# Performance work log

Measured on AMD Instinct MI355X. Metric: run time of the kernel, lower is better.

Reference implementation:

```python
import jax, jax.numpy as jnp
import numpy as np

B, S, D, H = 2, 2048, 1024, 16
DK = D // H


def setup_inputs() -> dict:
    key = jax.random.key(0)
    ks = jax.random.split(key, 12)
    scale = 1.0 / np.sqrt(D)
    inp = {
        "query": jax.random.normal(ks[0], (B, S, D), jnp.float32),
        "key": jax.random.normal(ks[1], (B, S, D), jnp.float32),
        "value": jax.random.normal(ks[2], (B, S, D), jnp.float32),
        "mask": jnp.broadcast_to(jnp.tril(jnp.ones((S, S), bool)), (B, S, S)),
        "Wq": jax.random.normal(ks[3], (D, D), jnp.float32) * scale,
        "bq": jnp.zeros((D,), jnp.float32),
        "Wk": jax.random.normal(ks[4], (D, D), jnp.float32) * scale,
        "bk": jnp.zeros((D,), jnp.float32),
        "Wv": jax.random.normal(ks[5], (D, D), jnp.float32) * scale,
        "bv": jnp.zeros((D,), jnp.float32),
        "Wo": jax.random.normal(ks[6], (D, D), jnp.float32) * scale,
        "bo": jnp.zeros((D,), jnp.float32),
    }
    return inp


def _split_heads(x):
    # [B, S, D] -> [B, H, S, DK]
    return x.reshape(B, S, H, DK).transpose(0, 2, 1, 3)


def reference(query, key, value, mask, Wq, bq, Wk, bk, Wv, bv, Wo, bo):
    q = _split_heads(query @ Wq + bq)
    k = _split_heads(key @ Wk + bk)
    v = _split_heads(value @ Wv + bv)
    # scores: [B, H, S, S]
    scores = jnp.einsum("bhqd,bhkd->bhqk", q, k) / jnp.sqrt(jnp.float32(DK))
    scores = jnp.where(mask[:, None, :, :], scores, jnp.float32(-1e9))
    p_attn = jax.nn.softmax(scores, axis=-1)
    x = jnp.einsum("bhqk,bhkd->bhqd", p_attn, v)  # [B, H, S, DK]
    x = x.transpose(0, 2, 1, 3).reshape(B, S, D)
    return x @ Wo + bo
```

## Files before the change

### kernel.cpp

```cpp
#include <hip/hip_runtime.h>


#define S_LEN 2048
#define DMODEL 1024
#define NHEAD 16
#define DKH 64
#define QSCALE 0.18033688011112042f

typedef __attribute__((ext_vector_type(8))) short short8;
typedef __attribute__((ext_vector_type(4))) float f32x4;
typedef __attribute__((ext_vector_type(4))) unsigned short ushort4v;

__device__ __forceinline__ unsigned short f2bf(float f) {
  union { float f; unsigned int u; } v; v.f = f;
  unsigned int r = v.u + 0x7fffu + ((v.u >> 16) & 1u);
  return (unsigned short)(r >> 16);
}

__device__ __forceinline__ void gload_lds16(const void* g, void* l) {
  __builtin_amdgcn_global_load_lds(
      (const __attribute__((address_space(1))) void*)g,
      (__attribute__((address_space(3))) void*)l, 16, 0, 0);
}

__global__ __launch_bounds__(256) void transpose_cast(const float* __restrict__ W,
                                                      unsigned short* __restrict__ Wt) {
  __shared__ float tile[32][33];
  const int tx = threadIdx.x, ty = threadIdx.y;
  const int c0 = blockIdx.x * 32, r0 = blockIdx.y * 32;
#pragma unroll
  for (int i = 0; i < 32; i += 8)
    tile[ty + i][tx] = W[(r0 + ty + i) * 1024 + c0 + tx];
  __syncthreads();
#pragma unroll
  for (int i = 0; i < 32; i += 8)
    Wt[(c0 + ty + i) * 1024 + r0 + tx] = f2bf(tile[tx][ty + i]);
}

__global__ __launch_bounds__(256) void cast3(const float* __restrict__ s0,
                                             const float* __restrict__ s1,
                                             const float* __restrict__ s2,
                                             unsigned short* __restrict__ d0,
                                             unsigned short* __restrict__ d1,
                                             unsigned short* __restrict__ d2) {
  const int z = blockIdx.y;
  const float* src = (z == 0) ? s0 : (z == 1) ? s1 : s2;
  unsigned short* dst = (z == 0) ? d0 : (z == 1) ? d1 : d2;
  const int i = (blockIdx.x * 256 + threadIdx.x) * 8;
  float4 a = *(const float4*)&src[i];
  float4 b = *(const float4*)&src[i + 4];
  unsigned short u[8];
  u[0] = f2bf(a.x); u[1] = f2bf(a.y); u[2] = f2bf(a.z); u[3] = f2bf(a.w);
  u[4] = f2bf(b.x); u[5] = f2bf(b.y); u[6] = f2bf(b.z); u[7] = f2bf(b.w);
  *(short8*)&dst[i] = *(short8*)u;
}

__global__ __launch_bounds__(256) void qkv_gemm(
    const unsigned short* Qc, const unsigned short* Kc, const unsigned short* Vc,
    const unsigned short* WtQ, const unsigned short* WtK, const unsigned short* WtV,
    const float* bq, const float* bk, const float* bv,
    unsigned short* Qw, unsigned short* Kw, unsigned short* Vtw) {
  __shared__ unsigned short Alds[2][4096];
  __shared__ unsigned short Blds[2][4096];
  const int z = blockIdx.z;
  const unsigned short* A  = (z == 0) ? Qc : (z == 1) ? Kc : Vc;
  const unsigned short* Wt = (z == 0) ? WtQ : (z == 1) ? WtK : WtV;
  const float* bias        = (z == 0) ? bq : (z == 1) ? bk : bv;

  const int tid = threadIdx.x;
  const int m0 = blockIdx.x * 128, n0 = blockIdx.y * 128;
  const int wid = tid >> 6, lane = tid & 63;
  const int lg = lane >> 4, lr = lane & 15;
  const int wr = (wid >> 1) * 64, wc = (wid & 1) * 64;
  const int srow_base = wid * 32 + (lane >> 2);
  const int scol = (lane & 3) * 8;

  f32x4 acc[4][4] = {};

#define GSTAGE(BUF, KT)                                                          \
  {                                                                              \
    _Pragma("unroll")                                                            \
    for (int i = 0; i < 2; i++) {                                                \
      const int row = srow_base + i * 16;                                        \
      gload_lds16(A  + (m0 + row) * 1024 + (KT) + scol,                          \
                  (char*)&Alds[BUF][0] + wid * 2048 + i * 1024);                 \
      gload_lds16(Wt + (n0 + row) * 1024 + (KT) + scol,                          \
                  (char*)&Blds[BUF][0] + wid * 2048 + i * 1024);                 \
    }                                                                            \
  }

  GSTAGE(0, 0)
  int cur = 0;
  for (int kt = 0; kt < 1024; kt += 32) {
    __syncthreads();
    if (kt + 32 < 1024) GSTAGE(cur ^ 1, kt + 32)
    short8 af[4], bfr[4];
#pragma unroll
    for (int i = 0; i < 4; i++) af[i] = *(short8*)&Alds[cur][(wr + i * 16 + lr) * 32 + lg * 8];
#pragma unroll
    for (int i = 0; i < 4; i++) bfr[i] = *(short8*)&Blds[cur][(wc + i * 16 + lr) * 32 + lg * 8];
#pragma unroll
    for (int mi = 0; mi < 4; mi++)
#pragma unroll
      for (int ni = 0; ni < 4; ni++)
        acc[mi][ni] = __builtin_amdgcn_mfma_f32_16x16x32_bf16(af[mi], bfr[ni], acc[mi][ni], 0, 0, 0);
    cur ^= 1;
  }
#undef GSTAGE

  if (z < 2) {
    unsigned short* O = (z == 0) ? Qw : Kw;
    const float sc = (z == 0) ? QSCALE : 1.0f;
#pragma unroll
    for (int mi = 0; mi < 4; mi++)
#pragma unroll
      for (int ni = 0; ni < 4; ni++) {
        const int gn = n0 + wc + ni * 16 + lr;
        const int h = gn >> 6, dk = gn & 63;
        const float bb = bias[gn];
#pragma unroll
        for (int r = 0; r < 4; r++) {
          const int gm = m0 + wr + mi * 16 + lg * 4 + r;
          const int b = gm >> 11, s = gm & 2047;
          O[(((b * NHEAD + h) * S_LEN + s) << 6) + dk] = f2bf((acc[mi][ni][r] + bb) * sc);
        }
      }
  } else {
#pragma unroll
    for (int mi = 0; mi < 4; mi++)
#pragma unroll
      for (int ni = 0; ni < 4; ni++) {
        const int gn = n0 + wc + ni * 16 + lr;
        const int h = gn >> 6, dk = gn & 63;
        const float bb = bias[gn];
        const int gm = m0 + wr + mi * 16 + lg * 4;
        const int b = gm >> 11, s = gm & 2047;
        unsigned short u[4];
#pragma unroll
        for (int r = 0; r < 4; r++) u[r] = f2bf(acc[mi][ni][r] + bb);
        *(ushort4v*)&Vtw[(((b * NHEAD + h) * DKH + dk) << 11) + s] = *(ushort4v*)u;
      }
  }
}

__global__ __launch_bounds__(256) void oproj_gemm(const unsigned short* __restrict__ A,
                                                  const unsigned short* __restrict__ Wt,
                                                  const float* __restrict__ bias,
                                                  float* __restrict__ Of32) {
  __shared__ unsigned short Alds[2][2048];
  __shared__ unsigned short Blds[2][4096];
  const int tid = threadIdx.x;
  const int m0 = blockIdx.x * 64, n0 = blockIdx.y * 128;
  const int wid = tid >> 6, lane = tid & 63;
  const int lg = lane >> 4, lr = lane & 15;
  const int wc = wid * 32;
  const int arow = wid * 16 + (lane >> 2);
  const int brow_base = wid * 32 + (lane >> 2);
  const int scol = (lane & 3) * 8;

  f32x4 acc[4][2] = {};

#define OSTAGE(BUF, KT)                                                          \
  {                                                                              \
    gload_lds16(A + (m0 + arow) * 1024 + (KT) + scol,                            \
                (char*)&Alds[BUF][0] + wid * 1024);                              \
    _Pragma("unroll")                                                            \
    for (int i = 0; i < 2; i++) {                                                \
      const int row = brow_base + i * 16;                                        \
      gload_lds16(Wt + (n0 + row) * 1024 + (KT) + scol,                          \
                  (char*)&Blds[BUF][0] + wid * 2048 + i * 1024);                 \
    }                                                                            \
  }

  OSTAGE(0, 0)
  int cur = 0;
  for (int kt = 0; kt < 1024; kt += 32) {
    __syncthreads();
    if (kt + 32 < 1024) OSTAGE(cur ^ 1, kt + 32)
    short8 af[4], bfr[2];
#pragma unroll
    for (int i = 0; i < 4; i++) af[i] = *(short8*)&Alds[cur][(i * 16 + lr) * 32 + lg * 8];
#pragma unroll
    for (int j = 0; j < 2; j++) bfr[j] = *(short8*)&Blds[cur][(wc + j * 16 + lr) * 32 + lg * 8];
#pragma unroll
    for (int mi = 0; mi < 4; mi++)
#pragma unroll
      for (int ni = 0; ni < 2; ni++)
        acc[mi][ni] = __builtin_amdgcn_mfma_f32_16x16x32_bf16(af[mi], bfr[ni], acc[mi][ni], 0, 0, 0);
    cur ^= 1;
  }
#undef OSTAGE

#pragma unroll
  for (int mi = 0; mi < 4; mi++)
#pragma unroll
    for (int ni = 0; ni < 2; ni++) {
      const int gn = n0 + wc + ni * 16 + lr;
      const float bb = bias[gn];
#pragma unroll
      for (int r = 0; r < 4; r++) {
        const int gm = m0 + mi * 16 + lg * 4 + r;
        Of32[gm * 1024 + gn] = acc[mi][ni][r] + bb;
      }
    }
}

__global__ __launch_bounds__(256) void attn_k(const unsigned short* __restrict__ Q,
                                              const unsigned short* __restrict__ K,
                                              const unsigned short* __restrict__ Vt,
                                              unsigned short* __restrict__ X) {
  __shared__ unsigned short Kb[2][4096];
  __shared__ unsigned short Vb[2][4096];
  __shared__ unsigned short Plds[4][16][72];
  const int tid = threadIdx.x;
  const int wid = tid >> 6, lane = tid & 63;
  const int lg = lane >> 4, lr = lane & 15;
  const int bh = blockIdx.y;
  const unsigned short* Qh = Q + bh * (S_LEN * DKH);
  const char* KhB = (const char*)(K + bh * (S_LEN * DKH));
  const char* VtB = (const char*)(Vt + bh * (DKH * S_LEN));
  const int b = bh >> 4, h = bh & 15;

  const int srow_lo = (lane >> 3);
  const int scolb = (lane & 7) * 16;

  short8 ones8;
#pragma unroll
  for (int i = 0; i < 8; i++) ones8[i] = (short)0x3F80;

  for (int pass = 0; pass < 2; ++pass) {
    const int qt = (pass == 0) ? (int)blockIdx.x : 31 - (int)blockIdx.x;
    const int qr = qt * 64 + wid * 16;

    short8 qf[2];
#pragma unroll
    for (int c = 0; c < 2; c++) qf[c] = *(const short8*)&Qh[(qr + lr) * 64 + c * 32 + lg * 8];

    f32x4 o[4] = {};
    f32x4 lsv = {};

    int cur = 0;
    __syncthreads();

#define STAGE(BUF, KV)                                                          \
    {                                                                           \
      _Pragma("unroll")                                                         \
      for (int i = 0; i < 2; i++) {                                             \
        const int row = wid * 16 + i * 8 + srow_lo;                             \
        const int sw = scolb ^ ((row & 7) << 4);                                \
        gload_lds16(KhB + ((KV) + row) * 128 + sw,                              \
                    (char*)&Kb[BUF][0] + wid * 2048 + i * 1024);                \
        gload_lds16(VtB + row * 4096 + (KV) * 2 + sw,                           \
                    (char*)&Vb[BUF][0] + wid * 2048 + i * 1024);                \
      }                                                                         \
    }

    STAGE(cur, 0);

    for (int t = 0; t <= qt; ++t) {
      __syncthreads();
      if (t < qt) STAGE(cur ^ 1, (t + 1) * 64);
      const int kv = t * 64;
      const bool diag = (t == qt);

      f32x4 sa[4] = {};
      __builtin_amdgcn_s_setprio(1);
#pragma unroll
      for (int jf = 0; jf < 4; jf++) {
        const int row = jf * 16 + lr;
#pragma unroll
        for (int c = 0; c < 2; c++) {
          const int cb = (c * 64 + lg * 16) ^ ((lr & 7) << 4);
          short8 kf = *(const short8*)((const char*)&Kb[cur][0] + row * 128 + cb);
          sa[jf] = __builtin_amdgcn_mfma_f32_16x16x32_bf16(qf[c], kf, sa[jf], 0, 0, 0);
        }
      }
      __builtin_amdgcn_s_setprio(0);

#pragma unroll
      for (int jf = 0; jf < 4; jf++) {
        const int j = kv + jf * 16 + lr;
#pragma unroll
        for (int r = 0; r < 4; r++) {
          float s = sa[jf][r];
          if (diag) s = (j > qr + lg * 4 + r) ? -1e30f : s;
          Plds[wid][lg * 4 + r][jf * 16 + lr] = f2bf(exp2f(s));
        }
      }
      short8 pa[2];
#pragma unroll
      for (int c = 0; c < 2; c++) pa[c] = *(short8*)&Plds[wid][lr][c * 32 + lg * 8];
      __builtin_amdgcn_s_setprio(1);
#pragma unroll
      for (int f = 0; f < 4; f++) {
        const int row = f * 16 + lr;
#pragma unroll
        for (int c = 0; c < 2; c++) {
          const int cb = (c * 64 + lg * 16) ^ ((lr & 7) << 4);
          short8 vf = *(const short8*)((const char*)&Vb[cur][0] + row * 128 + cb);
          o[f] = __builtin_amdgcn_mfma_f32_16x16x32_bf16(pa[c], vf, o[f], 0, 0, 0);
        }
      }
#pragma unroll
      for (int c = 0; c < 2; c++)
        lsv = __builtin_amdgcn_mfma_f32_16x16x32_bf16(pa[c], ones8, lsv, 0, 0, 0);
      __builtin_amdgcn_s_setprio(0);
      cur ^= 1;
    }

#pragma unroll
    for (int r = 0; r < 4; r++) {
      const float inv = 1.f / lsv[r];
      const int q = qr + lg * 4 + r;
#pragma unroll
      for (int f = 0; f < 4; f++)
        X[(b * S_LEN + q) * DMODEL + h * DKH + f * 16 + lr] = f2bf(o[f][r] * inv);
    }
  }
#undef STAGE
}

extern "C" void kernel_launch(void* const* d_in, const int* in_sizes, int n_in,
                              void* d_out, int out_size, void* d_ws, size_t ws_size,
                              hipStream_t stream) {
  const float* query = (const float*)d_in[0];
  const float* key   = (const float*)d_in[1];
  const float* value = (const float*)d_in[2];
  const float* Wq = (const float*)d_in[4];
  const float* bq = (const float*)d_in[5];
  const float* Wk = (const float*)d_in[6];
  const float* bk = (const float*)d_in[7];
  const float* Wv = (const float*)d_in[8];
  const float* bv = (const float*)d_in[9];
  const float* Wo = (const float*)d_in[10];
  const float* bo = (const float*)d_in[11];
  float* out = (float*)d_out;

  unsigned short* ws = (unsigned short*)d_ws;
  unsigned short* WtQ = ws;
  unsigned short* WtK = ws + 1048576;
  unsigned short* WtV = ws + 2097152;
  unsigned short* WtO = ws + 3145728;
  unsigned short* Qw  = ws + 4194304;
  unsigned short* Kw  = ws + 8388608;
  unsigned short* Vtw = ws + 12582912;
  unsigned short* Xw  = ws + 16777216;
  unsigned short* Qc  = ws + 20971520;
  unsigned short* Kc  = ws + 25165824;
  unsigned short* Vc  = ws + 29360128;
  (void)in_sizes; (void)n_in; (void)out_size; (void)ws_size;

  dim3 tb(32, 8), tg(32, 32);
  transpose_cast<<<tg, tb, 0, stream>>>(Wq, WtQ);
  transpose_cast<<<tg, tb, 0, stream>>>(Wk, WtK);
  transpose_cast<<<tg, tb, 0, stream>>>(Wv, WtV);
  transpose_cast<<<tg, tb, 0, stream>>>(Wo, WtO);

  cast3<<<dim3(2048, 3), 256, 0, stream>>>(query, key, value, Qc, Kc, Vc);

  qkv_gemm<<<dim3(32, 8, 3), 256, 0, stream>>>(Qc, Kc, Vc, WtQ, WtK, WtV,
                                               bq, bk, bv, Qw, Kw, Vtw);

  attn_k<<<dim3(16, 32), 256, 0, stream>>>(Qw, Kw, Vtw, Xw);

  oproj_gemm<<<dim3(64, 8), 256, 0, stream>>>(Xw, WtO, bo, out);
}
```

Before: 141.9 us.

## Keep attention probabilities in registers by transposing QK^T MFMA operands

Swaps the A/B operands of the QK^T MFMA so each lane holds score values along the key dimension, which lets the P fragment be packed directly into MFMA A-operand registers with v_cvt_pk_bf16_f32. This removes the per-tile LDS round trip through the Plds buffer and the scalar f2bf conversions. The V fragment reads are reorganised into two 8-byte loads to match the new k-index permutation. The causal mask is now applied as zeroing after exp2 only on diagonal tiles, and the reliance on a consistent permutation between the P and V operands adds correctness risk.

```diff
diff --git a/kernel.cpp b/kernel.cpp
--- a/kernel.cpp
+++ b/kernel.cpp
@@ -8,6 +8,7 @@
 #define QSCALE 0.18033688011112042f
 
 typedef __attribute__((ext_vector_type(8))) short short8;
+typedef __attribute__((ext_vector_type(4))) short short4v;
 typedef __attribute__((ext_vector_type(4))) float f32x4;
 typedef __attribute__((ext_vector_type(4))) unsigned short ushort4v;
 
@@ -15,6 +16,12 @@
   union { float f; unsigned int u; } v; v.f = f;
   unsigned int r = v.u + 0x7fffu + ((v.u >> 16) & 1u);
   return (unsigned short)(r >> 16);
+}
+
+__device__ __forceinline__ unsigned int cvtpk_bf16(float lo, float hi) {
+  unsigned int d;
+  asm("v_cvt_pk_bf16_f32 %0, %1, %2" : "=v"(d) : "v"(lo), "v"(hi));
+  return d;
 }
 
 __device__ __forceinline__ void gload_lds16(const void* g, void* l) {
@@ -211,7 +218,6 @@
                                               unsigned short* __restrict__ X) {
   __shared__ unsigned short Kb[2][4096];
   __shared__ unsigned short Vb[2][4096];
-  __shared__ unsigned short Plds[4][16][72];
   const int tid = threadIdx.x;
   const int wid = tid >> 6, lane = tid & 63;
   const int lg = lane >> 4, lr = lane & 15;
@@ -260,7 +266,6 @@
     for (int t = 0; t <= qt; ++t) {
       __syncthreads();
       if (t < qt) STAGE(cur ^ 1, (t + 1) * 64);
-      const int kv = t * 64;
       const bool diag = (t == qt);
 
       f32x4 sa[4] = {};
@@ -272,38 +277,53 @@
         for (int c = 0; c < 2; c++) {
           const int cb = (c * 64 + lg * 16) ^ ((lr & 7) << 4);
           short8 kf = *(const short8*)((const char*)&Kb[cur][0] + row * 128 + cb);
-          sa[jf] = __builtin_amdgcn_mfma_f32_16x16x32_bf16(qf[c], kf, sa[jf], 0, 0, 0);
+          sa[jf] = __builtin_amdgcn_mfma_f32_16x16x32_bf16(kf, qf[c], sa[jf], 0, 0, 0);
         }
       }
       __builtin_amdgcn_s_setprio(0);
 
-#pragma unroll
-      for (int jf = 0; jf < 4; jf++) {
-        const int j = kv + jf * 16 + lr;
-#pragma unroll
-        for (int r = 0; r < 4; r++) {
-          float s = sa[jf][r];
-          if (diag) s = (j > qr + lg * 4 + r) ? -1e30f : s;
-          Plds[wid][lg * 4 + r][jf * 16 + lr] = f2bf(exp2f(s));
+      float p[4][4];
+      if (diag) {
+        const int qloc = wid * 16 + lr;
+#pragma unroll
+        for (int jf = 0; jf < 4; jf++)
+#pragma unroll
+          for (int r = 0; r < 4; r++) {
+            const float e = exp2f(sa[jf][r]);
+            p[jf][r] = (jf * 16 + lg * 4 + r > qloc) ? 0.f : e;
+          }
+      } else {
+#pragma unroll
+        for (int jf = 0; jf < 4; jf++)
+#pragma unroll
+          for (int r = 0; r < 4; r++) p[jf][r] = exp2f(sa[jf][r]);
+      }
+
+      union { short8 v; unsigned int u[4]; } pk[2];
+#pragma unroll
+      for (int c = 0; c < 2; c++) {
+        pk[c].u[0] = cvtpk_bf16(p[2 * c][0], p[2 * c][1]);
+        pk[c].u[1] = cvtpk_bf16(p[2 * c][2], p[2 * c][3]);
+        pk[c].u[2] = cvtpk_bf16(p[2 * c + 1][0], p[2 * c + 1][1]);
+        pk[c].u[3] = cvtpk_bf16(p[2 * c + 1][2], p[2 * c + 1][3]);
+      }
+
+      __builtin_amdgcn_s_setprio(1);
+#pragma unroll
+      for (int f = 0; f < 4; f++) {
+        const char* vrow = (const char*)&Vb[cur][0] + (f * 16 + lr) * 128;
+        const int swz = (lr & 7) << 4;
+#pragma unroll
+        for (int c = 0; c < 2; c++) {
+          union { short8 v; short4v h[2]; } vv;
+          vv.h[0] = *(const short4v*)(vrow + ((c * 64 + lg * 8) ^ swz));
+          vv.h[1] = *(const short4v*)(vrow + ((c * 64 + 32 + lg * 8) ^ swz));
+          o[f] = __builtin_amdgcn_mfma_f32_16x16x32_bf16(pk[c].v, vv.v, o[f], 0, 0, 0);
         }
       }
-      short8 pa[2];
-#pragma unroll
-      for (int c = 0; c < 2; c++) pa[c] = *(short8*)&Plds[wid][lr][c * 32 + lg * 8];
-      __builtin_amdgcn_s_setprio(1);
-#pragma unroll
-      for (int f = 0; f < 4; f++) {
-        const int row = f * 16 + lr;
-#pragma unroll
-        for (int c = 0; c < 2; c++) {
-          const int cb = (c * 64 + lg * 16) ^ ((lr & 7) << 4);
-          short8 vf = *(const short8*)((const char*)&Vb[cur][0] + row * 128 + cb);
-          o[f] = __builtin_amdgcn_mfma_f32_16x16x32_bf16(pa[c], vf, o[f], 0, 0, 0);
-        }
-      }
 #pragma unroll
       for (int c = 0; c < 2; c++)
-        lsv = __builtin_amdgcn_mfma_f32_16x16x32_bf16(pa[c], ones8, lsv, 0, 0, 0);
+        lsv = __builtin_amdgcn_mfma_f32_16x16x32_bf16(pk[c].v, ones8, lsv, 0, 0, 0);
       __builtin_amdgcn_s_setprio(0);
       cur ^= 1;
     }
```

Measured after the change: 140.8 us. About the same (-0.8%).
